# Performance work log

Hardware: AMD Instinct MI355X
Metric: run time of the kernel (lower is better)

Reference implementation:

```python
import jax, jax.numpy as jnp
import numpy as np

NEG = -9e15

def setup_inputs() -> dict:
    key = jax.random.key(0)
    k1, k2, k3, k4, k5 = jax.random.split(key, 5)
    N, Fin, Fout = 8192, 256, 128
    h = jax.random.normal(k1, (N, Fin), dtype=jnp.float32)
    adj = jax.random.randint(k2, (N, N), 0, 2, dtype=jnp.int32)
    # Parameters (xavier_uniform with gain=1.414 for a1/a2; kaiming-like for W is fine as random init)
    lim_w = float(np.sqrt(6.0 / (Fin + Fout)))
    W = jax.random.uniform(k3, (Fout, Fin), dtype=jnp.float32, minval=-lim_w, maxval=lim_w)
    lim_a = float(1.414 * np.sqrt(6.0 / (Fout + 1)))
    a1 = jax.random.uniform(k4, (Fout, 1), dtype=jnp.float32, minval=-lim_a, maxval=lim_a)
    a2 = jax.random.uniform(k5, (Fout, 1), dtype=jnp.float32, minval=-lim_a, maxval=lim_a)
    return {"h": h, "adj": adj, "W": W, "a1": a1, "a2": a2}

def reference(h, adj, W, a1, a2):
    Wh = h @ W.T                                   # [N, Fout]
    s1 = (Wh @ a1)                                 # [N, 1]
    s2 = (Wh @ a2)                                 # [N, 1]
    e = jax.nn.leaky_relu(s1 + s2.T, 0.2)          # [N, N]
    att = jnp.where(adj > 0, e, jnp.float32(NEG))
    att = jax.nn.softmax(att, axis=1)
    h_prime = att @ Wh                             # [N, Fout]
    return jax.nn.elu(h_prime)
```

## Files before the change

### kernel.cpp

```cpp
#include <hip/hip_runtime.h>
#include <cstdint>
#include <cstddef>

#define N_NODES 8192
#define FIN 256
#define FOUT 128
#define JS 8
#define JW (N_NODES / JS)
#define KCH (JW / 32)
#define LOG2E 1.4426950408889634f

typedef __attribute__((ext_vector_type(8))) short bf16x8;
typedef __attribute__((ext_vector_type(4))) float f32x4;
typedef __attribute__((ext_vector_type(4))) int i32x4;

__device__ __forceinline__ float bf2f(unsigned short u) {
    union { unsigned int i; float f; } v; v.i = ((unsigned int)u) << 16; return v.f;
}
__device__ __forceinline__ unsigned short f2bf(float f) {
    union { float f; unsigned int i; } v; v.f = f;
    unsigned int r = (v.i + 0x7FFFu + ((v.i >> 16) & 1u)) >> 16;
    return (unsigned short)r;
}
__device__ __forceinline__ unsigned int pack_bf16(float a, float b) {
    return (unsigned)f2bf(a) | ((unsigned)f2bf(b) << 16);
}

__device__ __forceinline__ size_t whb_idx(int j, int f) {
    return ((size_t)((j >> 5) * 8 + (f >> 4)) << 9) + (((j >> 3) & 3) << 7)
         + ((f & 15) << 3) + (j & 7);
}

__global__ __launch_bounds__(256) void wh_kernel(const float* __restrict__ h,
                                                 const float* __restrict__ W,
                                                 unsigned short* __restrict__ whB) {
    __shared__ float hT[64][FIN + 5];
    const int t = threadIdx.x;
    const int i0 = blockIdx.x * 64;
    const int f0 = blockIdx.y * 32;
#pragma unroll
    for (int c = 0; c < 16; ++c) {
        int chunk = c * 256 + t;
        int row = chunk >> 6, col = (chunk & 63) * 4;
        f32x4 v = *(const f32x4*)&h[(size_t)(i0 + row) * FIN + col];
        hT[row][col] = v[0]; hT[row][col + 1] = v[1];
        hT[row][col + 2] = v[2]; hT[row][col + 3] = v[3];
    }
    __syncthreads();
    const int lane = t & 63;
    const int fb8 = __builtin_amdgcn_readfirstlane(f0 + (t >> 6) * 8);
    const float* w0 = W + (size_t)fb8 * FIN;
    float acc[8] = {0.f, 0.f, 0.f, 0.f, 0.f, 0.f, 0.f, 0.f};
    for (int k = 0; k < FIN; k += 4) {
        float h0 = hT[lane][k],     h1 = hT[lane][k + 1];
        float h2 = hT[lane][k + 2], h3 = hT[lane][k + 3];
#pragma unroll
        for (int c = 0; c < 8; ++c) {
            const float* wr = w0 + c * FIN;
            acc[c] += h0 * wr[k] + h1 * wr[k + 1] + h2 * wr[k + 2] + h3 * wr[k + 3];
        }
    }
    const int i = i0 + lane;
#pragma unroll
    for (int c = 0; c < 8; ++c)
        whB[whb_idx(i, fb8 + c)] = f2bf(acc[c]);
}

__global__ __launch_bounds__(256) void s_kernel(const unsigned short* __restrict__ whB,
                                                const float* __restrict__ a1,
                                                const float* __restrict__ a2,
                                                float* __restrict__ s1,
                                                float* __restrict__ s2) {
    __shared__ float p1[4][64], p2[4][64];
    const int t = threadIdx.x;
    const int l = t & 63;
    const int g = t >> 6;
    const int i = blockIdx.x * 64 + l;
    float acc1 = 0.f, acc2 = 0.f;
#pragma unroll
    for (int fb = g * 2; fb < g * 2 + 2; ++fb) {
#pragma unroll
        for (int sl = 0; sl < 16; ++sl) {
            int f = fb * 16 + sl;
            float v = bf2f(whB[whb_idx(i, f)]);
            acc1 += v * a1[f];
            acc2 += v * a2[f];
        }
    }
    p1[g][l] = acc1; p2[g][l] = acc2;
    __syncthreads();
    if (g == 0) {
        s1[i] = (p1[0][l] + p1[1][l] + p1[2][l] + p1[3][l]) * LOG2E;
        s2[i] = (p2[0][l] + p2[1][l] + p2[2][l] + p2[3][l]) * LOG2E;
    }
}

__global__ __launch_bounds__(256) void gat_kernel(const int* __restrict__ adj,
                                                  const unsigned short* __restrict__ whB,
                                                  const float* __restrict__ s1,
                                                  const float* __restrict__ s2,
                                                  float* __restrict__ out,
                                                  float* __restrict__ nums,
                                                  float* __restrict__ dens) {
    const int t = threadIdx.x;
    const int w = t >> 6;
    const int lane = t & 63;
    const int sl = lane & 15;
    const int quad = lane >> 4;
    const int slice = blockIdx.x & (JS - 1);
    const int rg = (blockIdx.x >> 3) * 4 + w;
    const int row0 = rg * 32;
    const int jb = slice * JW;
    float* __restrict__ num = slice ? (nums + (size_t)(slice - 1) * N_NODES * FOUT) : out;
    float* __restrict__ den = dens + (size_t)slice * N_NODES;

    const float s1a = s1[row0 + sl];
    const float s1b = s1[row0 + 16 + sl];
    const int* aR0 = adj + (size_t)(row0 + sl) * N_NODES + jb + quad * 8;
    const int* aR1 = aR0 + (size_t)16 * N_NODES;
    const float* s2p = s2 + jb + quad * 8;

    f32x4 acc[2][8];
#pragma unroll
    for (int m = 0; m < 2; ++m)
#pragma unroll
        for (int fb = 0; fb < 8; ++fb) acc[m][fb] = (f32x4){0.f, 0.f, 0.f, 0.f};

    float d0 = 0.f, d1 = 0.f;

    i32x4 pa0 = *(const i32x4*)(aR0);
    i32x4 pa1 = *(const i32x4*)(aR0 + 4);
    i32x4 pb0 = *(const i32x4*)(aR1);
    i32x4 pb1 = *(const i32x4*)(aR1 + 4);
    f32x4 ps0 = *(const f32x4*)(s2p);
    f32x4 ps1 = *(const f32x4*)(s2p + 4);

#pragma unroll 1
    for (int ch = 0; ch < KCH; ++ch) {
        i32x4 ca0 = pa0, ca1 = pa1, cb0 = pb0, cb1 = pb1;
        f32x4 cs0 = ps0, cs1 = ps1;
        if (ch + 1 < KCH) {
            int o = (ch + 1) * 32;
            pa0 = *(const i32x4*)(aR0 + o);
            pa1 = *(const i32x4*)(aR0 + o + 4);
            pb0 = *(const i32x4*)(aR1 + o);
            pb1 = *(const i32x4*)(aR1 + o + 4);
            ps0 = *(const f32x4*)(s2p + o);
            ps1 = *(const f32x4*)(s2p + o + 4);
        }
        const int kb = jb / 32 + ch;
        const unsigned short* bp = whB + ((size_t)(kb * 8) << 9) + lane * 8;
        bf16x8 B[8];
#pragma unroll
        for (int fb = 0; fb < 8; ++fb) B[fb] = *(const bf16x8*)(bp + ((size_t)fb << 9));
        float p0[8], p1[8];
#pragma unroll
        for (int e = 0; e < 8; ++e) {
            float sc = (e < 4) ? cs0[e] : cs1[e - 4];
            int m0 = (e < 4) ? ca0[e] : ca1[e - 4];
            int m1 = (e < 4) ? cb0[e] : cb1[e - 4];
            float y0 = s1a + sc;
            float y1 = s1b + sc;
            y0 = fmaxf(y0, 0.2f * y0);
            y1 = fmaxf(y1, 0.2f * y1);
            float e0 = __builtin_amdgcn_exp2f(y0);
            float e1 = __builtin_amdgcn_exp2f(y1);
            p0[e] = (m0 > 0) ? e0 : 0.f;
            p1[e] = (m1 > 0) ? e1 : 0.f;
            d0 += p0[e];
            d1 += p1[e];
        }
        union { bf16x8 v; unsigned int u[4]; } A0, A1;
#pragma unroll
        for (int q = 0; q < 4; ++q) {
            A0.u[q] = pack_bf16(p0[2 * q], p0[2 * q + 1]);
            A1.u[q] = pack_bf16(p1[2 * q], p1[2 * q + 1]);
        }
#pragma unroll
        for (int fb = 0; fb < 8; ++fb) {
            acc[0][fb] = __builtin_amdgcn_mfma_f32_16x16x32_bf16(A0.v, B[fb], acc[0][fb], 0, 0, 0);
            acc[1][fb] = __builtin_amdgcn_mfma_f32_16x16x32_bf16(A1.v, B[fb], acc[1][fb], 0, 0, 0);
        }
    }
    d0 += __shfl_xor(d0, 16); d0 += __shfl_xor(d0, 32);
    d1 += __shfl_xor(d1, 16); d1 += __shfl_xor(d1, 32);
    if (lane < 16) {
        den[row0 + lane] = d0;
        den[row0 + 16 + lane] = d1;
    }
#pragma unroll
    for (int m = 0; m < 2; ++m)
#pragma unroll
        for (int fb = 0; fb < 8; ++fb)
#pragma unroll
            for (int r = 0; r < 4; ++r) {
                int row = row0 + m * 16 + quad * 4 + r;
                num[(size_t)row * FOUT + fb * 16 + sl] = acc[m][fb][r];
            }
}

__global__ __launch_bounds__(256) void fin_kernel(float* __restrict__ out,
                                                  const float* __restrict__ nums,
                                                  const float* __restrict__ dens) {
    const int idx = blockIdx.x * 256 + threadIdx.x;
    const int i = idx >> 7;
    const size_t NF = (size_t)N_NODES * FOUT;
    float numv = out[idx];
#pragma unroll
    for (int k = 0; k < JS - 1; ++k) numv += nums[k * NF + idx];
    float denv = 0.f;
#pragma unroll
    for (int k = 0; k < JS; ++k) denv += dens[k * N_NODES + i];
    float v = numv / fmaxf(denv, 1e-30f);
    out[idx] = (v > 0.f) ? v : expm1f(v);
}

extern "C" void kernel_launch(void* const* d_in, const int* in_sizes, int n_in,
                              void* d_out, int out_size, void* d_ws, size_t ws_size,
                              hipStream_t stream) {
    const float* h   = (const float*)d_in[0];
    const int*   adj = (const int*)d_in[1];
    const float* W   = (const float*)d_in[2];
    const float* a1  = (const float*)d_in[3];
    const float* a2  = (const float*)d_in[4];

    char* ws = (char*)d_ws;
    unsigned short* whB = (unsigned short*)ws;
    float* s1   = (float*)(ws + (2u << 20));
    float* s2   = s1 + N_NODES;
    float* dens = s2 + N_NODES;
    float* nums = dens + JS * N_NODES;
    float* out  = (float*)d_out;

    wh_kernel<<<dim3(N_NODES / 64, FOUT / 32), 256, 0, stream>>>(h, W, whB);
    s_kernel<<<dim3(N_NODES / 64), 256, 0, stream>>>(whB, a1, a2, s1, s2);
    gat_kernel<<<dim3((N_NODES / 128) * JS), 256, 0, stream>>>(adj, whB, s1, s2,
                                                               out, nums, dens);
    fin_kernel<<<dim3(N_NODES * FOUT / 256), 256, 0, stream>>>(out, nums, dens);
}
```

Before: 446.1 us.

## Pack adjacency into transposed bitmasks and stage Wh tiles through LDS

Adds a pre-pass that compresses the int32 adjacency matrix into transposed 32-bit bitmasks using wave ballots. The attention kernel then reads one word per row per chunk instead of eight ints per lane. Wh B-tiles are also double-buffered into shared memory with global_load_lds, so the four waves in a block share one copy instead of each loading it separately. The pack pass still has to read the full 256MB adjacency once, and the new per-chunk __syncthreads adds synchronisation cost.

```diff
diff --git a/kernel.cpp b/kernel.cpp
--- a/kernel.cpp
+++ b/kernel.cpp
@@ -12,7 +12,6 @@
 
 typedef __attribute__((ext_vector_type(8))) short bf16x8;
 typedef __attribute__((ext_vector_type(4))) float f32x4;
-typedef __attribute__((ext_vector_type(4))) int i32x4;
 
 __device__ __forceinline__ float bf2f(unsigned short u) {
     union { unsigned int i; float f; } v; v.i = ((unsigned int)u) << 16; return v.f;
@@ -26,9 +25,34 @@
     return (unsigned)f2bf(a) | ((unsigned)f2bf(b) << 16);
 }
 
+__device__ __forceinline__ void stage16(const unsigned short* g, unsigned short* l) {
+    __builtin_amdgcn_global_load_lds(
+        (const __attribute__((address_space(1))) unsigned int*)g,
+        (__attribute__((address_space(3))) unsigned int*)l, 16, 0, 0);
+}
+
 __device__ __forceinline__ size_t whb_idx(int j, int f) {
     return ((size_t)((j >> 5) * 8 + (f >> 4)) << 9) + (((j >> 3) & 3) << 7)
          + ((f & 15) << 3) + (j & 7);
+}
+
+__global__ __launch_bounds__(256) void pack_kernel(const int* __restrict__ adj,
+                                                   unsigned int* __restrict__ bitsT) {
+    const int t = threadIdx.x;
+    const int lane = t & 63;
+    const int wv = t >> 6;
+    const int task = blockIdx.x * 4 + wv;
+    const int w = task & 127;
+    const int r0 = (task >> 7) * 64;
+    const int* ap = adj + (size_t)r0 * N_NODES + w * 64 + lane;
+    unsigned long long keep = 0;
+#pragma unroll
+    for (int r = 0; r < 64; ++r) {
+        unsigned long long m = __ballot(ap[(size_t)r * N_NODES] > 0);
+        if (lane == r) keep = m;
+    }
+    bitsT[(size_t)(2 * w) * N_NODES + r0 + lane]     = (unsigned int)keep;
+    bitsT[(size_t)(2 * w + 1) * N_NODES + r0 + lane] = (unsigned int)(keep >> 32);
 }
 
 __global__ __launch_bounds__(256) void wh_kernel(const float* __restrict__ h,
@@ -95,29 +119,30 @@
     }
 }
 
-__global__ __launch_bounds__(256) void gat_kernel(const int* __restrict__ adj,
+__global__ __launch_bounds__(256) void gat_kernel(const unsigned int* __restrict__ bitsT,
                                                   const unsigned short* __restrict__ whB,
                                                   const float* __restrict__ s1,
                                                   const float* __restrict__ s2,
                                                   float* __restrict__ out,
                                                   float* __restrict__ nums,
                                                   float* __restrict__ dens) {
+    __shared__ __align__(16) unsigned short lbuf[2][4096];
     const int t = threadIdx.x;
     const int w = t >> 6;
     const int lane = t & 63;
     const int sl = lane & 15;
     const int quad = lane >> 4;
     const int slice = blockIdx.x & (JS - 1);
-    const int rg = (blockIdx.x >> 3) * 4 + w;
-    const int row0 = rg * 32;
+    const int rb = blockIdx.x >> 3;
+    const int row0 = rb * 128 + w * 32;
     const int jb = slice * JW;
+    const int kb0 = slice * KCH;
     float* __restrict__ num = slice ? (nums + (size_t)(slice - 1) * N_NODES * FOUT) : out;
     float* __restrict__ den = dens + (size_t)slice * N_NODES;
 
     const float s1a = s1[row0 + sl];
     const float s1b = s1[row0 + 16 + sl];
-    const int* aR0 = adj + (size_t)(row0 + sl) * N_NODES + jb + quad * 8;
-    const int* aR1 = aR0 + (size_t)16 * N_NODES;
+    const unsigned int* bT = bitsT + (size_t)(jb >> 5) * N_NODES;
     const float* s2p = s2 + jb + quad * 8;
 
     f32x4 acc[2][8];
@@ -125,48 +150,47 @@
     for (int m = 0; m < 2; ++m)
 #pragma unroll
         for (int fb = 0; fb < 8; ++fb) acc[m][fb] = (f32x4){0.f, 0.f, 0.f, 0.f};
-
     float d0 = 0.f, d1 = 0.f;
 
-    i32x4 pa0 = *(const i32x4*)(aR0);
-    i32x4 pa1 = *(const i32x4*)(aR0 + 4);
-    i32x4 pb0 = *(const i32x4*)(aR1);
-    i32x4 pb1 = *(const i32x4*)(aR1 + 4);
-    f32x4 ps0 = *(const f32x4*)(s2p);
-    f32x4 ps1 = *(const f32x4*)(s2p + 4);
+    {
+        const unsigned short* gt = whB + ((size_t)((kb0) * 8 + 2 * w) << 9);
+        stage16(gt + lane * 8, &lbuf[0][2 * w * 512]);
+        stage16(gt + 512 + lane * 8, &lbuf[0][(2 * w + 1) * 512]);
+    }
+    unsigned int m0 = bT[(size_t)0 * N_NODES + row0 + sl];
+    unsigned int m1 = bT[(size_t)0 * N_NODES + row0 + 16 + sl];
+    f32x4 sv0 = *(const f32x4*)(s2p);
+    f32x4 sv1 = *(const f32x4*)(s2p + 4);
 
 #pragma unroll 1
     for (int ch = 0; ch < KCH; ++ch) {
-        i32x4 ca0 = pa0, ca1 = pa1, cb0 = pb0, cb1 = pb1;
-        f32x4 cs0 = ps0, cs1 = ps1;
+        __syncthreads();
+        unsigned int cm0 = m0 >> (quad * 8);
+        unsigned int cm1 = m1 >> (quad * 8);
+        f32x4 cs0 = sv0, cs1 = sv1;
         if (ch + 1 < KCH) {
+            const unsigned short* gt = whB + ((size_t)((kb0 + ch + 1) * 8 + 2 * w) << 9);
+            unsigned short* lb = &lbuf[(ch + 1) & 1][0];
+            stage16(gt + lane * 8, lb + 2 * w * 512);
+            stage16(gt + 512 + lane * 8, lb + (2 * w + 1) * 512);
+            m0 = bT[(size_t)(ch + 1) * N_NODES + row0 + sl];
+            m1 = bT[(size_t)(ch + 1) * N_NODES + row0 + 16 + sl];
             int o = (ch + 1) * 32;
-            pa0 = *(const i32x4*)(aR0 + o);
-            pa1 = *(const i32x4*)(aR0 + o + 4);
-            pb0 = *(const i32x4*)(aR1 + o);
-            pb1 = *(const i32x4*)(aR1 + o + 4);
-            ps0 = *(const f32x4*)(s2p + o);
-            ps1 = *(const f32x4*)(s2p + o + 4);
-        }
-        const int kb = jb / 32 + ch;
-        const unsigned short* bp = whB + ((size_t)(kb * 8) << 9) + lane * 8;
-        bf16x8 B[8];
-#pragma unroll
-        for (int fb = 0; fb < 8; ++fb) B[fb] = *(const bf16x8*)(bp + ((size_t)fb << 9));
+            sv0 = *(const f32x4*)(s2p + o);
+            sv1 = *(const f32x4*)(s2p + o + 4);
+        }
         float p0[8], p1[8];
 #pragma unroll
         for (int e = 0; e < 8; ++e) {
             float sc = (e < 4) ? cs0[e] : cs1[e - 4];
-            int m0 = (e < 4) ? ca0[e] : ca1[e - 4];
-            int m1 = (e < 4) ? cb0[e] : cb1[e - 4];
             float y0 = s1a + sc;
             float y1 = s1b + sc;
             y0 = fmaxf(y0, 0.2f * y0);
             y1 = fmaxf(y1, 0.2f * y1);
             float e0 = __builtin_amdgcn_exp2f(y0);
             float e1 = __builtin_amdgcn_exp2f(y1);
-            p0[e] = (m0 > 0) ? e0 : 0.f;
-            p1[e] = (m1 > 0) ? e1 : 0.f;
+            p0[e] = ((cm0 >> e) & 1u) ? e0 : 0.f;
+            p1[e] = ((cm1 >> e) & 1u) ? e1 : 0.f;
             d0 += p0[e];
             d1 += p1[e];
         }
@@ -176,10 +200,12 @@
             A0.u[q] = pack_bf16(p0[2 * q], p0[2 * q + 1]);
             A1.u[q] = pack_bf16(p1[2 * q], p1[2 * q + 1]);
         }
+        const unsigned short* lb = &lbuf[ch & 1][0];
 #pragma unroll
         for (int fb = 0; fb < 8; ++fb) {
-            acc[0][fb] = __builtin_amdgcn_mfma_f32_16x16x32_bf16(A0.v, B[fb], acc[0][fb], 0, 0, 0);
-            acc[1][fb] = __builtin_amdgcn_mfma_f32_16x16x32_bf16(A1.v, B[fb], acc[1][fb], 0, 0, 0);
+            bf16x8 B = *(const bf16x8*)(lb + fb * 512 + lane * 8);
+            acc[0][fb] = __builtin_amdgcn_mfma_f32_16x16x32_bf16(A0.v, B, acc[0][fb], 0, 0, 0);
+            acc[1][fb] = __builtin_amdgcn_mfma_f32_16x16x32_bf16(A1.v, B, acc[1][fb], 0, 0, 0);
         }
     }
     d0 += __shfl_xor(d0, 16); d0 += __shfl_xor(d0, 32);
@@ -225,16 +251,17 @@
     const float* a2  = (const float*)d_in[4];
 
     char* ws = (char*)d_ws;
-    unsigned short* whB = (unsigned short*)ws;
-    float* s1   = (float*)(ws + (2u << 20));
+    unsigned short* whB   = (unsigned short*)ws;
+    unsigned int*   bitsT = (unsigned int*)(ws + (2u << 20));
+    float* s1   = (float*)(ws + (10u << 20));
     float* s2   = s1 + N_NODES;
     float* dens = s2 + N_NODES;
     float* nums = dens + JS * N_NODES;
     float* out  = (float*)d_out;
 
+    pack_kernel<<<dim3(4096), 256, 0, stream>>>(adj, bitsT);
     wh_kernel<<<dim3(N_NODES / 64, FOUT / 32), 256, 0, stream>>>(h, W, whB);
     s_kernel<<<dim3(N_NODES / 64), 256, 0, stream>>>(whB, a1, a2, s1, s2);
-    gat_kernel<<<dim3((N_NODES / 128) * JS), 256, 0, stream>>>(adj, whB, s1, s2,
-                                                               out, nums, dens);
+    gat_kernel<<<dim3(64 * JS), 256, 0, stream>>>(bitsT, whB, s1, s2, out, nums, dens);
     fin_kernel<<<dim3(N_NODES * FOUT / 256), 256, 0, stream>>>(out, nums, dens);
 }
```

Result: no change. 440.3 us (-1.3%).
